# Kernel optimization log

Measured on AMD Instinct MI355X. Metric: run time of the kernel, lower is better.

Reference implementation:

```python
import jax, jax.numpy as jnp
import numpy as np

K = 20
EPS = 1e-5
SLOPE = 0.2


def knn(x, k=K):
    # x: (B, C, N); returns indices of k nearest neighbors (largest -dist^2), (B, N, k)
    xx = jnp.sum(x * x, axis=1)                      # (B, N)
    inner = jnp.einsum('bcn,bcm->bnm', x, x)         # (B, N, N)
    pd = 2.0 * inner - xx[:, :, None] - xx[:, None, :]  # -squared distance
    _, idx = jax.lax.top_k(pd, k)
    return idx


def graph_feature(x, idx):
    # x: (B, C, N), idx: (B, N, k) -> (B, 2C, N): concat(x, max_k(neighbor) - x)
    feat = jnp.transpose(x, (0, 2, 1))               # (B, N, C)
    nb = jax.vmap(lambda f, i: f[i])(feat, idx)      # (B, N, k, C)
    nb_max = nb.max(axis=2)                          # (B, N, C)
    out = jnp.concatenate([feat, nb_max - feat], axis=-1)  # (B, N, 2C)
    return jnp.transpose(out, (0, 2, 1))


def conv_bn_lrelu(x, W, g, b):
    # 1x1 Conv2d (no bias) on (B,C,N,1) == channel matmul; BN2d training-mode; LeakyReLU
    h = jnp.einsum('oc,bcn->bon', W, x)              # (B, O, N)
    mu = h.mean(axis=(0, 2), keepdims=True)
    var = h.var(axis=(0, 2), keepdims=True)
    h = (h - mu) / jnp.sqrt(var + EPS) * g[None, :, None] + b[None, :, None]
    return jax.nn.leaky_relu(h, SLOPE)


def bn1d_lrelu(h, g, b):
    mu = h.mean(axis=0, keepdims=True)
    var = h.var(axis=0, keepdims=True)
    h = (h - mu) / jnp.sqrt(var + EPS) * g[None, :] + b[None, :]
    return jax.nn.leaky_relu(h, SLOPE)


def forward(x, W1, g1, b1, W2, g2, b2, W3, g3, b3, W4, g4, b4, W5, g5, b5,
            L1, g6, b6, L2, bl2, g7, b7, L3, bl3):
    B = x.shape[0]
    idx = knn(x)                                      # knn on raw xyz
    h = conv_bn_lrelu(x, W1, g1, b1)                  # (B, 64, N)
    x1 = graph_feature(h, idx)                        # (B, 128, N)

    idx = knn(x1)
    h = conv_bn_lrelu(x1, W2, g2, b2)                 # (B, 64, N)
    x2 = graph_feature(h, idx)                        # (B, 128, N)

    idx = knn(x2)
    h = conv_bn_lrelu(x2, W3, g3, b3)                 # (B, 64, N)
    x3 = graph_feature(h, idx)                        # (B, 128, N)

    idx = knn(x3)
    h = conv_bn_lrelu(x3, W4, g4, b4)                 # (B, 128, N)
    x4 = graph_feature(h, idx)                        # (B, 256, N)

    xc = jnp.concatenate([x1, x2, x3, x4], axis=1)    # (B, 640, N)
    h5 = conv_bn_lrelu(xc, W5, g5, b5)                # (B, 1024, N)
    feat = h5.max(axis=1)                             # max over CHANNELS -> (B, N=1024)

    h = bn1d_lrelu(feat @ L1.T, g6, b6)               # (B, 512); dropout=identity (eval)
    h = bn1d_lrelu(h @ L2.T + bl2, g7, b7)            # (B, 256)
    return h @ L3.T + bl3                             # (B, 40)


def setup_inputs() -> dict:
    key = jax.random.key(0)
    ks = jax.random.split(key, 32)
    ki = iter(ks)

    def rn(shape, scale=0.1):
        return jax.random.normal(next(ki), shape, dtype=jnp.float32) * scale

    def bn_params(c):
        return 1.0 + rn((c,)), rn((c,))

    x = jax.random.normal(next(ki), (32, 3, 1024), dtype=jnp.float32)
    W1 = rn((64, 3));    g1, b1 = bn_params(64)
    W2 = rn((64, 128));  g2, b2 = bn_params(64)
    W3 = rn((64, 128));  g3, b3 = bn_params(64)
    W4 = rn((128, 128)); g4, b4 = bn_params(128)
    W5 = rn((1024, 640)); g5, b5 = bn_params(1024)
    L1 = rn((512, 1024)); g6, b6 = bn_params(512)
    L2 = rn((256, 512)); bl2 = rn((256,)); g7, b7 = bn_params(256)
    L3 = rn((40, 256));  bl3 = rn((40,))
    return dict(x=x, W1=W1, g1=g1, b1=b1, W2=W2, g2=g2, b2=b2, W3=W3, g3=g3, b3=b3,
                W4=W4, g4=g4, b4=b4, W5=W5, g5=g5, b5=b5, L1=L1, g6=g6, b6=b6,
                L2=L2, bl2=bl2, g7=g7, b7=b7, L3=L3, bl3=bl3)


def reference(x, W1, g1, b1, W2, g2, b2, W3, g3, b3, W4, g4, b4, W5, g5, b5,
              L1, g6, b6, L2, bl2, g7, b7, L3, bl3):
    return forward(x, W1, g1, b1, W2, g2, b2, W3, g3, b3, W4, g4, b4, W5, g5, b5,
                   L1, g6, b6, L2, bl2, g7, b7, L3, bl3)
```

## Files before the change

kernel.cpp:

```cpp
#include <hip/hip_runtime.h>
#include <cfloat>
#include <cstdint>

#define NB 32
#define NPTS 1024
#define KNN 20
#define RTOT (NB * NPTS)

typedef __attribute__((ext_vector_type(8))) short bf16x8;
typedef __attribute__((ext_vector_type(4))) float f32x4;

__device__ __forceinline__ float lrelu(float v) { return v >= 0.f ? v : 0.2f * v; }

__global__ void k_transpose_x(const float* __restrict__ x, float* __restrict__ xT) {
    int g = blockIdx.x * 256 + threadIdx.x;
    if (g >= NB * 3 * NPTS) return;
    int n = g % NPTS;
    int c = (g / NPTS) % 3;
    int b = g / (3 * NPTS);
    xT[((size_t)b * NPTS + n) * 3 + c] = x[g];
}

__global__ void k_xx(const float* __restrict__ X, int ldx, int C, float* __restrict__ xx) {
    int r = blockIdx.x * 256 + threadIdx.x;
    if (r >= RTOT) return;
    const float* p = X + (size_t)r * ldx;
    float s = 0.f;
    for (int c = 0; c < C; ++c) { float v = p[c]; s += v * v; }
    xx[r] = s;
}

__global__ __launch_bounds__(256) void k_gemm_xwt(
    const float* __restrict__ X, int ldx, int K,
    const float* __restrict__ W,
    float* __restrict__ H, int ldh)
{
    __shared__ float As[16][68];
    __shared__ float Bs[16][68];
    int tid = threadIdx.x;
    int tx = tid & 15, ty = tid >> 4;
    int c0 = blockIdx.x * 64;
    int r0 = blockIdx.y * 64;
    float acc[4][4] = {};
    int lr = tid >> 4, lk = tid & 15;
    for (int k0 = 0; k0 < K; k0 += 16) {
#pragma unroll
        for (int i = 0; i < 4; ++i) {
            int row = lr + i * 16;
            int kk = k0 + lk;
            float av = 0.f, bv = 0.f;
            if (kk < K) {
                av = X[(size_t)(r0 + row) * ldx + kk];
                bv = W[(size_t)(c0 + row) * K + kk];
            }
            As[lk][row] = av;
            Bs[lk][row] = bv;
        }
        __syncthreads();
#pragma unroll
        for (int k = 0; k < 16; ++k) {
            float4 a4 = *(const float4*)&As[k][ty * 4];
            float4 b4 = *(const float4*)&Bs[k][tx * 4];
            float av[4] = {a4.x, a4.y, a4.z, a4.w};
            float bv[4] = {b4.x, b4.y, b4.z, b4.w};
#pragma unroll
            for (int i = 0; i < 4; ++i)
#pragma unroll
                for (int j = 0; j < 4; ++j)
                    acc[i][j] = fmaf(av[i], bv[j], acc[i][j]);
        }
        __syncthreads();
    }
#pragma unroll
    for (int i = 0; i < 4; ++i) {
        float4 v = make_float4(acc[i][0], acc[i][1], acc[i][2], acc[i][3]);
        *(float4*)&H[(size_t)(r0 + ty * 4 + i) * ldh + c0 + tx * 4] = v;
    }
}

__global__ __launch_bounds__(256) void k_pd128(
    const float* __restrict__ X, int ldx, int K,
    const float* __restrict__ xx, float* __restrict__ pd)
{
    __shared__ float As[16][132];
    __shared__ float Bs[16][132];
    int b = blockIdx.z;
    int tid = threadIdx.x;
    int tx = tid & 15, ty = tid >> 4;
    int c0 = blockIdx.x * 128;
    int r0 = blockIdx.y * 128;
    const float* Xb = X + (size_t)b * NPTS * ldx;
    int lk = tid & 15, lr = tid >> 4;
    float acc[8][8] = {};
    for (int k0 = 0; k0 < K; k0 += 16) {
#pragma unroll
        for (int i = 0; i < 8; ++i) {
            int row = lr + i * 16;
            int kk = k0 + lk;
            float av = 0.f, bv = 0.f;
            if (kk < K) {
                av = Xb[(size_t)(r0 + row) * ldx + kk];
                bv = Xb[(size_t)(c0 + row) * ldx + kk];
            }
            As[lk][row] = av;
            Bs[lk][row] = bv;
        }
        __syncthreads();
#pragma unroll
        for (int k = 0; k < 16; ++k) {
            float a[8], bb[8];
            *(float4*)&a[0]  = *(const float4*)&As[k][ty * 4];
            *(float4*)&a[4]  = *(const float4*)&As[k][64 + ty * 4];
            *(float4*)&bb[0] = *(const float4*)&Bs[k][tx * 4];
            *(float4*)&bb[4] = *(const float4*)&Bs[k][64 + tx * 4];
#pragma unroll
            for (int i = 0; i < 8; ++i)
#pragma unroll
                for (int j = 0; j < 8; ++j)
                    acc[i][j] = fmaf(a[i], bb[j], acc[i][j]);
        }
        __syncthreads();
    }
    const float* xxb = xx + (size_t)b * NPTS;
    float* pdb = pd + (size_t)b * NPTS * NPTS;
    float xcA[4], xcB[4];
#pragma unroll
    for (int j = 0; j < 4; ++j) {
        xcA[j] = xxb[c0 + tx * 4 + j];
        xcB[j] = xxb[c0 + 64 + tx * 4 + j];
    }
#pragma unroll
    for (int i = 0; i < 8; ++i) {
        int r = r0 + ((i < 4) ? (ty * 4 + i) : (64 + ty * 4 + i - 4));
        float xr = xxb[r];
        float* orow = &pdb[(size_t)r * NPTS + c0];
        float4 v0, v1;
        v0.x = 2.f * acc[i][0] - xr - xcA[0];
        v0.y = 2.f * acc[i][1] - xr - xcA[1];
        v0.z = 2.f * acc[i][2] - xr - xcA[2];
        v0.w = 2.f * acc[i][3] - xr - xcA[3];
        v1.x = 2.f * acc[i][4] - xr - xcB[0];
        v1.y = 2.f * acc[i][5] - xr - xcB[1];
        v1.z = 2.f * acc[i][6] - xr - xcB[2];
        v1.w = 2.f * acc[i][7] - xr - xcB[3];
        *(float4*)&orow[tx * 4]      = v0;
        *(float4*)&orow[64 + tx * 4] = v1;
    }
}

__global__ __launch_bounds__(256) void k_topk_wave(const float* __restrict__ pd, int* __restrict__ idx) {
    int wid = (blockIdx.x * 256 + threadIdx.x) >> 6;
    int lane = threadIdx.x & 63;
    const float* row = pd + (size_t)wid * NPTS;
    float v[16];
#pragma unroll
    for (int j = 0; j < 16; ++j) v[j] = row[lane + 64 * j];
    float bv = v[0]; int bj = 0;
#pragma unroll
    for (int j = 1; j < 16; ++j) if (v[j] > bv) { bv = v[j]; bj = j; }
    int* out = idx + (size_t)wid * KNN;
    for (int kk = 0; kk < KNN; ++kk) {
        float cv = bv;
        int ci = lane + (bj << 6);
#pragma unroll
        for (int s = 1; s < 64; s <<= 1) {
            float ov = __shfl_xor(cv, s);
            int oi = __shfl_xor(ci, s);
            if (ov > cv || (ov == cv && oi < ci)) { cv = ov; ci = oi; }
        }
        if (lane == 0) out[kk] = ci;
        bool mine = (ci & 63) == lane;
        int jdead = ci >> 6;
#pragma unroll
        for (int j = 0; j < 16; ++j) if (mine && j == jdead) v[j] = -FLT_MAX;
        bv = v[0]; bj = 0;
#pragma unroll
        for (int j = 1; j < 16; ++j) if (v[j] > bv) { bv = v[j]; bj = j; }
    }
}

__device__ __forceinline__ void split2(float x, ushort& h, ushort& l) {
    uint u = __float_as_uint(x);
    uint r = u + 0x7FFFu + ((u >> 16) & 1u);
    ushort hh = (ushort)(r >> 16);
    float hf = __uint_as_float((uint)hh << 16);
    float d = x - hf;
    uint u2 = __float_as_uint(d);
    uint r2 = u2 + 0x7FFFu + ((u2 >> 16) & 1u);
    h = hh;
    l = (ushort)(r2 >> 16);
}

__device__ __forceinline__ uint pack2(ushort a, ushort b) { return (uint)a | ((uint)b << 16); }

__device__ __forceinline__ void stage_split(const float* __restrict__ g,
                                            ushort* __restrict__ dh, ushort* __restrict__ dl) {
    float4 v0 = *(const float4*)(g);
    float4 v1 = *(const float4*)(g + 4);
    float4 v2 = *(const float4*)(g + 8);
    float4 v3 = *(const float4*)(g + 12);
    float xs[16] = {v0.x, v0.y, v0.z, v0.w, v1.x, v1.y, v1.z, v1.w,
                    v2.x, v2.y, v2.z, v2.w, v3.x, v3.y, v3.z, v3.w};
    ushort h[16], l[16];
#pragma unroll
    for (int i = 0; i < 16; ++i) split2(xs[i], h[i], l[i]);
    uint4 H0, H1, L0, L1;
    H0.x = pack2(h[0], h[1]);  H0.y = pack2(h[2], h[3]);
    H0.z = pack2(h[4], h[5]);  H0.w = pack2(h[6], h[7]);
    H1.x = pack2(h[8], h[9]);  H1.y = pack2(h[10], h[11]);
    H1.z = pack2(h[12], h[13]); H1.w = pack2(h[14], h[15]);
    L0.x = pack2(l[0], l[1]);  L0.y = pack2(l[2], l[3]);
    L0.z = pack2(l[4], l[5]);  L0.w = pack2(l[6], l[7]);
    L1.x = pack2(l[8], l[9]);  L1.y = pack2(l[10], l[11]);
    L1.z = pack2(l[12], l[13]); L1.w = pack2(l[14], l[15]);
    *(uint4*)(dh)     = H0;
    *(uint4*)(dh + 8) = H1;
    *(uint4*)(dl)     = L0;
    *(uint4*)(dl + 8) = L1;
}

#define LDK 40
__global__ __launch_bounds__(256) void k_gemm5_mfma(
    const float* __restrict__ X, const float* __restrict__ W, float* __restrict__ H)
{
    __shared__ __align__(16) ushort sAh[128 * LDK];
    __shared__ __align__(16) ushort sAl[128 * LDK];
    __shared__ __align__(16) ushort sBh[128 * LDK];
    __shared__ __align__(16) ushort sBl[128 * LDK];
    int tid = threadIdx.x;
    int lane = tid & 63, w = tid >> 6;
    int wm = w >> 1, wn = w & 1;
    int r0 = blockIdx.y * 128, c0 = blockIdx.x * 128;
    int srow = tid >> 1, sk = (tid & 1) * 16;
    int fr = lane & 15;
    int kg = (lane >> 4) << 3;
    f32x4 acc[4][4] = {};
    for (int k0 = 0; k0 < 640; k0 += 32) {
        stage_split(X + (size_t)(r0 + srow) * 640 + k0 + sk,
                    &sAh[srow * LDK + sk], &sAl[srow * LDK + sk]);
        stage_split(W + (size_t)(c0 + srow) * 640 + k0 + sk,
                    &sBh[srow * LDK + sk], &sBl[srow * LDK + sk]);
        __syncthreads();
        bf16x8 ah[4], al[4];
#pragma unroll
        for (int mi = 0; mi < 4; ++mi) {
            int rr = wm * 64 + mi * 16 + fr;
            ah[mi] = *(const bf16x8*)&sAh[rr * LDK + kg];
            al[mi] = *(const bf16x8*)&sAl[rr * LDK + kg];
        }
#pragma unroll
        for (int ni = 0; ni < 4; ++ni) {
            int cc = wn * 64 + ni * 16 + fr;
            bf16x8 bh = *(const bf16x8*)&sBh[cc * LDK + kg];
            bf16x8 bl = *(const bf16x8*)&sBl[cc * LDK + kg];
#pragma unroll
            for (int mi = 0; mi < 4; ++mi) {
                acc[mi][ni] = __builtin_amdgcn_mfma_f32_16x16x32_bf16(ah[mi], bh, acc[mi][ni], 0, 0, 0);
                acc[mi][ni] = __builtin_amdgcn_mfma_f32_16x16x32_bf16(ah[mi], bl, acc[mi][ni], 0, 0, 0);
                acc[mi][ni] = __builtin_amdgcn_mfma_f32_16x16x32_bf16(al[mi], bh, acc[mi][ni], 0, 0, 0);
            }
        }
        __syncthreads();
    }
#pragma unroll
    for (int mi = 0; mi < 4; ++mi) {
        int rg = r0 + wm * 64 + mi * 16 + (lane >> 4) * 4;
#pragma unroll
        for (int ni = 0; ni < 4; ++ni) {
            int cg = c0 + wn * 64 + ni * 16 + fr;
#pragma unroll
            for (int r = 0; r < 4; ++r)
                H[(size_t)(rg + r) * 1024 + cg] = acc[mi][ni][r];
        }
    }
}

__global__ __launch_bounds__(256) void k_bn_stats(const float* __restrict__ H, int ldh, int O, int R,
                                                  float* __restrict__ sums) {
    int nblk = gridDim.x;
    int rows = (R + nblk - 1) / nblk;
    int r0 = blockIdx.x * rows;
    int r1 = r0 + rows; if (r1 > R) r1 = R;
    int tid = threadIdx.x;
    if (O <= 256) {
        int per = 256 / O;
        int c = tid % O;
        int rOff = tid / O;
        float s = 0.f, s2 = 0.f;
        for (int r = r0 + rOff; r < r1; r += per) {
            float v = H[(size_t)r * ldh + c];
            s += v; s2 += v * v;
        }
        __shared__ float ls[256], ls2[256];
        ls[tid] = s; ls2[tid] = s2;
        __syncthreads();
        for (int st = 128; st >= O; st >>= 1) {
            if (tid < st) { ls[tid] += ls[tid + st]; ls2[tid] += ls2[tid + st]; }
            __syncthreads();
        }
        if (tid < O) {
            atomicAdd(&sums[c], ls[tid]);
            atomicAdd(&sums[O + c], ls2[tid]);
        }
    } else {
        int nc = O / 256;
        float s[4] = {0, 0, 0, 0}, s2[4] = {0, 0, 0, 0};
        for (int r = r0; r < r1; ++r) {
            const float* rowp = H + (size_t)r * ldh;
            for (int i = 0; i < nc; ++i) {
                float v = rowp[tid + i * 256];
                s[i] += v; s2[i] += v * v;
            }
        }
        for (int i = 0; i < nc; ++i) {
            atomicAdd(&sums[tid + i * 256], s[i]);
            atomicAdd(&sums[O + tid + i * 256], s2[i]);
        }
    }
}

__global__ void k_bn_finalize(const float* __restrict__ sums, const float* __restrict__ g,
                              const float* __restrict__ bta, int O, float invR,
                              float* __restrict__ ss) {
    int o = blockIdx.x * 256 + threadIdx.x;
    if (o >= O) return;
    float mu = sums[o] * invR;
    float var = sums[O + o] * invR - mu * mu;
    float sc = g[o] / sqrtf(var + 1e-5f);
    ss[o] = sc;
    ss[O + o] = bta[o] - mu * sc;
}

__global__ __launch_bounds__(256) void k_graph_feature(
    const float* __restrict__ hT, int ldh, int C,
    const int* __restrict__ idx, const float* __restrict__ ss,
    float* __restrict__ out, int ldo, int colOff)
{
    int ppb = 256 / C;
    int p = threadIdx.x / C;
    int c = threadIdx.x % C;
    int r = blockIdx.x * ppb + p;
    int b = r >> 10;
    float sc = ss[c], sh = ss[C + c];
    float self = hT[(size_t)r * ldh + c];
    float vs = lrelu(sc * self + sh);
    const int* ip = idx + (size_t)r * KNN;
    float m = -FLT_MAX;
#pragma unroll 4
    for (int k = 0; k < KNN; ++k) {
        int j = ip[k];
        float hv = hT[((size_t)b * NPTS + j) * ldh + c];
        float v = lrelu(sc * hv + sh);
        m = fmaxf(m, v);
    }
    float* orow = out + (size_t)r * ldo + colOff;
    orow[c] = vs;
    orow[C + c] = m - vs;
}

__global__ __launch_bounds__(256) void k_chanmax(const float* __restrict__ h5,
                                                 const float* __restrict__ ss,
                                                 float* __restrict__ feat) {
    int r = blockIdx.x;
    int tid = threadIdx.x;
    __shared__ float red[256];
    const float* rowp = h5 + (size_t)r * 1024;
    float m = -FLT_MAX;
    for (int o = tid; o < 1024; o += 256) {
        float v = lrelu(ss[o] * rowp[o] + ss[1024 + o]);
        m = fmaxf(m, v);
    }
    red[tid] = m;
    __syncthreads();
    for (int s = 128; s > 0; s >>= 1) {
        if (tid < s) red[tid] = fmaxf(red[tid], red[tid + s]);
        __syncthreads();
    }
    if (tid == 0) feat[r] = red[0];
}

__global__ void k_fc(const float* __restrict__ in, const float* __restrict__ Lw,
                     const float* __restrict__ bias, float* __restrict__ out, int K, int J) {
    int g = blockIdx.x * 256 + threadIdx.x;
    if (g >= 32 * J) return;
    int b = g / J, j = g % J;
    const float* xr = in + (size_t)b * K;
    const float* wr = Lw + (size_t)j * K;
    float acc = 0.f;
    for (int k = 0; k < K; ++k) acc = fmaf(xr[k], wr[k], acc);
    out[g] = bias ? acc + bias[j] : acc;
}

__global__ void k_bn1d(float* __restrict__ h, const float* __restrict__ g,
                       const float* __restrict__ bta, int J) {
    int j = blockIdx.x * 256 + threadIdx.x;
    if (j >= J) return;
    float s = 0.f, s2 = 0.f;
    for (int b = 0; b < 32; ++b) {
        float v = h[b * J + j];
        s += v; s2 += v * v;
    }
    float mu = s / 32.f;
    float var = s2 / 32.f - mu * mu;
    float sc = g[j] / sqrtf(var + 1e-5f);
    float sh = bta[j] - mu * sc;
    for (int b = 0; b < 32; ++b) {
        float v = sc * h[b * J + j] + sh;
        h[b * J + j] = lrelu(v);
    }
}

extern "C" void kernel_launch(void* const* d_in, const int* in_sizes, int n_in,
                              void* d_out, int out_size, void* d_ws, size_t ws_size,
                              hipStream_t stream) {
    const float* x   = (const float*)d_in[0];
    const float* W1  = (const float*)d_in[1];
    const float* g1  = (const float*)d_in[2];
    const float* b1  = (const float*)d_in[3];
    const float* W2  = (const float*)d_in[4];
    const float* g2  = (const float*)d_in[5];
    const float* b2  = (const float*)d_in[6];
    const float* W3  = (const float*)d_in[7];
    const float* g3  = (const float*)d_in[8];
    const float* b3  = (const float*)d_in[9];
    const float* W4  = (const float*)d_in[10];
    const float* g4  = (const float*)d_in[11];
    const float* b4  = (const float*)d_in[12];
    const float* W5  = (const float*)d_in[13];
    const float* g5  = (const float*)d_in[14];
    const float* b5  = (const float*)d_in[15];
    const float* L1  = (const float*)d_in[16];
    const float* g6  = (const float*)d_in[17];
    const float* b6  = (const float*)d_in[18];
    const float* L2  = (const float*)d_in[19];
    const float* bl2 = (const float*)d_in[20];
    const float* g7  = (const float*)d_in[21];
    const float* b7  = (const float*)d_in[22];
    const float* L3  = (const float*)d_in[23];
    const float* bl3 = (const float*)d_in[24];

    float* ws = (float*)d_ws;
    size_t off = 0;
    auto alloc = [&](size_t n) { size_t o = off; off += (n + 63) & ~(size_t)63; return o; };
    float* pd   = ws + alloc((size_t)NB * NPTS * NPTS);
    float* h5   = pd;
    float* xcT  = ws + alloc((size_t)RTOT * 640);
    float* hbuf = ws + alloc((size_t)RTOT * 128);
    float* xT   = ws + alloc((size_t)RTOT * 3);
    float* xxb  = ws + alloc(RTOT);
    float* sums = ws + alloc(2048);
    float* ss   = ws + alloc(2048);
    float* feat = ws + alloc(RTOT);
    float* h1   = ws + alloc(32 * 512);
    float* h2   = ws + alloc(32 * 256);
    int*   idxb = (int*)(ws + alloc((size_t)RTOT * KNN));

    k_transpose_x<<<(NB * 3 * NPTS + 255) / 256, 256, 0, stream>>>(x, xT);

    auto run_knn = [&](const float* X, int ldx, int C) {
        k_xx<<<(RTOT + 255) / 256, 256, 0, stream>>>(X, ldx, C, xxb);
        k_pd128<<<dim3(NPTS / 128, NPTS / 128, NB), 256, 0, stream>>>(X, ldx, C, xxb, pd);
        k_topk_wave<<<RTOT / 4, 256, 0, stream>>>(pd, idxb);
    };
    auto run_conv = [&](const float* X, int ldx, int K, const float* W,
                        const float* g, const float* bta, int O) {
        k_gemm_xwt<<<dim3(O / 64, RTOT / 64), 256, 0, stream>>>(X, ldx, K, W, hbuf, O);
        hipMemsetAsync(sums, 0, 2 * O * sizeof(float), stream);
        k_bn_stats<<<256, 256, 0, stream>>>(hbuf, O, O, RTOT, sums);
        k_bn_finalize<<<(O + 255) / 256, 256, 0, stream>>>(sums, g, bta, O, 1.f / RTOT, ss);
    };
    auto run_gf = [&](int C, int colOff) {
        int ppb = 256 / C;
        k_graph_feature<<<RTOT / ppb, 256, 0, stream>>>(hbuf, C, C, idxb, ss, xcT, 640, colOff);
    };

    run_knn(xT, 3, 3);
    run_conv(xT, 3, 3, W1, g1, b1, 64);
    run_gf(64, 0);

    run_knn(xcT + 0, 640, 128);
    run_conv(xcT + 0, 640, 128, W2, g2, b2, 64);
    run_gf(64, 128);

    run_knn(xcT + 128, 640, 128);
    run_conv(xcT + 128, 640, 128, W3, g3, b3, 64);
    run_gf(64, 256);

    run_knn(xcT + 256, 640, 128);
    run_conv(xcT + 256, 640, 128, W4, g4, b4, 128);
    run_gf(128, 384);

    k_gemm5_mfma<<<dim3(1024 / 128, RTOT / 128), 256, 0, stream>>>(xcT, W5, h5);
    hipMemsetAsync(sums, 0, 2048 * sizeof(float), stream);
    k_bn_stats<<<256, 256, 0, stream>>>(h5, 1024, 1024, RTOT, sums);
    k_bn_finalize<<<4, 256, 0, stream>>>(sums, g5, b5, 1024, 1.f / RTOT, ss);
    k_chanmax<<<RTOT, 256, 0, stream>>>(h5, ss, feat);

    k_fc<<<(32 * 512 + 255) / 256, 256, 0, stream>>>(feat, L1, nullptr, h1, 1024, 512);
    k_bn1d<<<(512 + 255) / 256, 256, 0, stream>>>(h1, g6, b6, 512);
    k_fc<<<(32 * 256 + 255) / 256, 256, 0, stream>>>(h1, L2, bl2, h2, 512, 256);
    k_bn1d<<<(256 + 255) / 256, 256, 0, stream>>>(h2, g7, b7, 256);
    k_fc<<<(32 * 40 + 255) / 256, 256, 0, stream>>>(h2, L3, bl3, (float*)d_out, 256, 40);
}
```

Before: 1.959 ms.

## Fuse BN stats into conv5 GEMM, pre-split W5, remap block order

A new kernel splits W5 into bf16 high and low halves once per call, so the conv5 GEMM loads them directly instead of re-splitting weights in every tile. The per-channel sum and sum-of-squares BN statistics are accumulated in the GEMM epilogue with shared and global atomics, which removes the separate k_bn_stats pass over the 32K×1024 output. Blocks are launched on a 1D grid and remapped with (bid&7)*256+(bid>>3), which changes which tiles run close together and may affect L2 reuse. The costs are an extra small kernel launch, float atomics whose order is not deterministic, and the split weight buffers.

Result: faster. 1.828 ms (-6.7%).

```diff
diff --git a/kernel.cpp b/kernel.cpp
--- a/kernel.cpp
+++ b/kernel.cpp
@@ -219,9 +219,29 @@
     *(uint4*)(dl + 8) = L1;
 }
 
+__global__ void k_split(const float* __restrict__ X, ushort* __restrict__ Xh,
+                        ushort* __restrict__ Xl, int n) {
+    int g = (blockIdx.x * 256 + threadIdx.x) * 8;
+    if (g >= n) return;
+    float4 a = *(const float4*)(X + g);
+    float4 b = *(const float4*)(X + g + 4);
+    float xs[8] = {a.x, a.y, a.z, a.w, b.x, b.y, b.z, b.w};
+    ushort h[8], l[8];
+#pragma unroll
+    for (int i = 0; i < 8; ++i) split2(xs[i], h[i], l[i]);
+    uint4 H, L;
+    H.x = pack2(h[0], h[1]); H.y = pack2(h[2], h[3]);
+    H.z = pack2(h[4], h[5]); H.w = pack2(h[6], h[7]);
+    L.x = pack2(l[0], l[1]); L.y = pack2(l[2], l[3]);
+    L.z = pack2(l[4], l[5]); L.w = pack2(l[6], l[7]);
+    *(uint4*)(Xh + g) = H;
+    *(uint4*)(Xl + g) = L;
+}
+
 #define LDK 40
 __global__ __launch_bounds__(256) void k_gemm5_mfma(
-    const float* __restrict__ X, const float* __restrict__ W, float* __restrict__ H)
+    const float* __restrict__ X, const ushort* __restrict__ Wh, const ushort* __restrict__ Wl,
+    float* __restrict__ H, float* __restrict__ sums)
 {
     __shared__ __align__(16) ushort sAh[128 * LDK];
     __shared__ __align__(16) ushort sAl[128 * LDK];
@@ -230,7 +250,10 @@
     int tid = threadIdx.x;
     int lane = tid & 63, w = tid >> 6;
     int wm = w >> 1, wn = w & 1;
-    int r0 = blockIdx.y * 128, c0 = blockIdx.x * 128;
+    int bid = blockIdx.x;
+    int wg = (bid & 7) * 256 + (bid >> 3);
+    int cb = wg & 7, rb = wg >> 3;
+    int r0 = rb * 128, c0 = cb * 128;
     int srow = tid >> 1, sk = (tid & 1) * 16;
     int fr = lane & 15;
     int kg = (lane >> 4) << 3;
@@ -238,8 +261,13 @@
     for (int k0 = 0; k0 < 640; k0 += 32) {
         stage_split(X + (size_t)(r0 + srow) * 640 + k0 + sk,
                     &sAh[srow * LDK + sk], &sAl[srow * LDK + sk]);
-        stage_split(W + (size_t)(c0 + srow) * 640 + k0 + sk,
-                    &sBh[srow * LDK + sk], &sBl[srow * LDK + sk]);
+        {
+            size_t gb = (size_t)(c0 + srow) * 640 + k0 + sk;
+            *(uint4*)&sBh[srow * LDK + sk]     = *(const uint4*)(Wh + gb);
+            *(uint4*)&sBh[srow * LDK + sk + 8] = *(const uint4*)(Wh + gb + 8);
+            *(uint4*)&sBl[srow * LDK + sk]     = *(const uint4*)(Wl + gb);
+            *(uint4*)&sBl[srow * LDK + sk + 8] = *(const uint4*)(Wl + gb + 8);
+        }
         __syncthreads();
         bf16x8 ah[4], al[4];
 #pragma unroll
@@ -272,6 +300,26 @@
             for (int r = 0; r < 4; ++r)
                 H[(size_t)(rg + r) * 1024 + cg] = acc[mi][ni][r];
         }
+    }
+    float* csum  = (float*)sAh;
+    float* csum2 = csum + 128;
+    if (tid < 128) { csum[tid] = 0.f; csum2[tid] = 0.f; }
+    __syncthreads();
+#pragma unroll
+    for (int ni = 0; ni < 4; ++ni) {
+        float s = 0.f, s2 = 0.f;
+#pragma unroll
+        for (int mi = 0; mi < 4; ++mi)
+#pragma unroll
+            for (int r = 0; r < 4; ++r) { float v = acc[mi][ni][r]; s += v; s2 += v * v; }
+        int c = wn * 64 + ni * 16 + fr;
+        atomicAdd(&csum[c], s);
+        atomicAdd(&csum2[c], s2);
+    }
+    __syncthreads();
+    if (tid < 128) {
+        atomicAdd(&sums[c0 + tid], csum[tid]);
+        atomicAdd(&sums[1024 + c0 + tid], csum2[tid]);
     }
 }
 
@@ -454,8 +502,11 @@
     float* h1   = ws + alloc(32 * 512);
     float* h2   = ws + alloc(32 * 256);
     int*   idxb = (int*)(ws + alloc((size_t)RTOT * KNN));
+    ushort* W5h = (ushort*)(ws + alloc(1024 * 640 / 2));
+    ushort* W5l = (ushort*)(ws + alloc(1024 * 640 / 2));
 
     k_transpose_x<<<(NB * 3 * NPTS + 255) / 256, 256, 0, stream>>>(x, xT);
+    k_split<<<(1024 * 640 / 8 + 255) / 256, 256, 0, stream>>>(W5, W5h, W5l, 1024 * 640);
 
     auto run_knn = [&](const float* X, int ldx, int C) {
         k_xx<<<(RTOT + 255) / 256, 256, 0, stream>>>(X, ldx, C, xxb);
@@ -490,9 +541,8 @@
     run_conv(xcT + 256, 640, 128, W4, g4, b4, 128);
     run_gf(128, 384);
 
-    k_gemm5_mfma<<<dim3(1024 / 128, RTOT / 128), 256, 0, stream>>>(xcT, W5, h5);
     hipMemsetAsync(sums, 0, 2048 * sizeof(float), stream);
-    k_bn_stats<<<256, 256, 0, stream>>>(h5, 1024, 1024, RTOT, sums);
+    k_gemm5_mfma<<<2048, 256, 0, stream>>>(xcT, W5h, W5l, h5, sums);
     k_bn_finalize<<<4, 256, 0, stream>>>(sums, g5, b5, 1024, 1.f / RTOT, ss);
     k_chanmax<<<RTOT, 256, 0, stream>>>(h5, ss, feat);
 
```
